# Optimization experiments

Hardware: AMD Instinct MI355X
Metric: run time of the kernel (lower is better)

Reference implementation:

```python
import jax, jax.numpy as jnp
import numpy as np

EMB = 1024
HEAD = 64
RANK = 8
LRA_SCL = 2.0
LORA = 1.0


def setup_inputs() -> dict:
    key = jax.random.key(0)
    ks = jax.random.split(key, 12)
    s = 1.0 / np.sqrt(EMB)
    sr = 1.0 / np.sqrt(RANK)
    inp = {
        "batEmb": jax.random.normal(ks[0], (8, 2048, EMB), dtype=jnp.float32),
        "tokMrk": jax.random.randint(ks[1], (8, 2048), 0, 2, dtype=jnp.int32),
        # base projections, nn.Linear weight layout [out, in]
        "Wq": jax.random.uniform(ks[2], (HEAD, EMB), jnp.float32, -s, s),
        "Wk": jax.random.uniform(ks[3], (HEAD, EMB), jnp.float32, -s, s),
        "Wv": jax.random.uniform(ks[4], (HEAD, EMB), jnp.float32, -s, s),
        # LoRA: A [rank, emb], B [head, rank]. (Original inits B to zero; we
        # randomize with small scale so the LoRA path is numerically exercised.)
        "Aq": jax.random.uniform(ks[5], (RANK, EMB), jnp.float32, -s, s),
        "Bq": jax.random.uniform(ks[6], (HEAD, RANK), jnp.float32, -sr, sr) * 0.02,
        "Ak": jax.random.uniform(ks[7], (RANK, EMB), jnp.float32, -s, s),
        "Bk": jax.random.uniform(ks[8], (HEAD, RANK), jnp.float32, -sr, sr) * 0.02,
        "Av": jax.random.uniform(ks[9], (RANK, EMB), jnp.float32, -s, s),
        "Bv": jax.random.uniform(ks[10], (HEAD, RANK), jnp.float32, -sr, sr) * 0.02,
    }
    return inp


def _proj(x, W, A, B):
    # base + LoRA low-rank delta (dropout = identity in eval)
    base = jnp.einsum('bse,he->bsh', x, W)
    lora = jnp.einsum('bsr,hr->bsh', jnp.einsum('bse,re->bsr', x, A), B)
    return base + lora * (LRA_SCL * LORA)


def reference(batEmb, tokMrk, Wq, Wk, Wv, Aq, Bq, Ak, Bk, Av, Bv):
    q = _proj(batEmb, Wq, Aq, Bq)  # [B,S,H]
    k = _proj(batEmb, Wk, Ak, Bk)
    v = _proj(batEmb, Wv, Av, Bv)
    w = jnp.einsum('bqh,bkh->bqk', q, k) * (HEAD ** -0.5)  # [B,S,S]
    mask = (tokMrk == 0)[:, None, :]  # [B,1,S] over key dim
    w = jnp.where(mask, -jnp.inf, w)
    w = jax.nn.softmax(w, axis=-1)
    w = jnp.nan_to_num(w, nan=0.0)
    return jnp.einsum('bqk,bkh->bqh', w, v)
```

## Files before the change

### kernel.cpp

```cpp
#include <hip/hip_runtime.h>
#include <hip/hip_bf16.h>
#include <stdint.h>

#define EMB 1024
#define NB 8
#define SEQ 2048
#define RANK 8
#define SPLIT 4

#define BM 64
#define BK 64
#define NSTG 16
#define BUFB 32768
#define NBUF 3

typedef __attribute__((ext_vector_type(8))) short bf16x8;
typedef __attribute__((ext_vector_type(4))) float f32x4;
typedef unsigned short u16;
typedef unsigned int u32;

__device__ __forceinline__ u16 f2bf(float f) {
  u32 u = __builtin_bit_cast(u32, f);
  u = (u + 0x7fffu + ((u >> 16) & 1u)) >> 16;
  return (u16)u;
}
__device__ __forceinline__ u32 pk2(float lo, float hi) {
  return (u32)f2bf(lo) | ((u32)f2bf(hi) << 16);
}
__device__ __forceinline__ void gll16(const void* g, void* l) {
  __builtin_amdgcn_global_load_lds(
      (const __attribute__((address_space(1))) unsigned int*)g,
      (__attribute__((address_space(3))) unsigned int*)l, 16, 0, 0);
}

#define PBAR()   asm volatile("s_barrier" ::: "memory")
#define WAITV(n) asm volatile("s_waitcnt vmcnt(" #n ")" ::: "memory")
#define WAITL()  asm volatile("s_waitcnt lgkmcnt(0)" ::: "memory")

__global__ __launch_bounds__(256) void fold_k(
    const float* __restrict__ Wq, const float* __restrict__ Wk, const float* __restrict__ Wv,
    const float* __restrict__ Aq, const float* __restrict__ Bq,
    const float* __restrict__ Ak, const float* __restrict__ Bk,
    const float* __restrict__ Av, const float* __restrict__ Bv,
    u16* __restrict__ weff) {
  int m = blockIdx.x;
  int mat = m >> 6, h = m & 63;
  const float* W = mat == 0 ? Wq : (mat == 1 ? Wk : Wv);
  const float* A = mat == 0 ? Aq : (mat == 1 ? Ak : Av);
  const float* B = mat == 0 ? Bq : (mat == 1 ? Bk : Bv);
  float bb[RANK];
#pragma unroll
  for (int r = 0; r < RANK; r++) bb[r] = 2.0f * B[h * RANK + r];
  int e = threadIdx.x * 4;
  float4 w4 = *(const float4*)(W + h * EMB + e);
  float a0 = w4.x, a1 = w4.y, a2 = w4.z, a3 = w4.w;
#pragma unroll
  for (int r = 0; r < RANK; r++) {
    float4 av = *(const float4*)(A + r * EMB + e);
    a0 += bb[r] * av.x; a1 += bb[r] * av.y; a2 += bb[r] * av.z; a3 += bb[r] * av.w;
  }
  u16* o = weff + (size_t)m * EMB + e;
  o[0] = f2bf(a0); o[1] = f2bf(a1); o[2] = f2bf(a2); o[3] = f2bf(a3);
}

__global__ __launch_bounds__(512) void proj_k(
    const float* __restrict__ X, const u16* __restrict__ weff,
    u16* __restrict__ qws, u16* __restrict__ kws, u16* __restrict__ vws) {
  extern __shared__ __align__(16) char smem[];

  int t = threadIdx.x;
  int w = t >> 6, l = t & 63;
  int rbase = blockIdx.x * BM;

  if (w >= 6) {
    int q = w - 6;
    int p = q * 64 + l;
    int xrow = p & 63;
    int xh = p >> 6;
    const float* xsrc = X + (size_t)(rbase + xrow) * EMB + xh * 8;
    int wkoff = ((l & 7) ^ (l >> 3)) << 3;
    int wc0 = l >> 3;

    float4 xr0[8], xr1[8];

#define ISSUE_X(st, xr) do {                                              \
    const float* s_ = xsrc + (st) * BK;                                   \
    _Pragma("unroll")                                                     \
    for (int wi_ = 0; wi_ < 4; wi_++) {                                   \
      xr[wi_*2]   = *(const float4*)(s_ + wi_ * 16);                      \
      xr[wi_*2+1] = *(const float4*)(s_ + wi_ * 16 + 4);                  \
    } } while (0)

#define WRITE_X(bufp, xr) do {                                            \
    _Pragma("unroll")                                                     \
    for (int wi_ = 0; wi_ < 4; wi_++) {                                   \
      uint4 v_;                                                           \
      v_.x = pk2(xr[wi_*2].x,   xr[wi_*2].y);                             \
      v_.y = pk2(xr[wi_*2].z,   xr[wi_*2].w);                             \
      v_.z = pk2(xr[wi_*2+1].x, xr[wi_*2+1].y);                           \
      v_.w = pk2(xr[wi_*2+1].z, xr[wi_*2+1].w);                           \
      *(uint4*)((bufp) + (wi_*2 + xh) * 1024 + xrow * 16) = v_;           \
    } } while (0)

#define ISSUE_W(st, bufp) do {                                            \
    _Pragma("unroll")                                                     \
    for (int i_ = 0; i_ < 12; i_++) { int wj_ = q * 12 + i_;              \
      gll16(weff + (size_t)(wj_ * 8 + wc0) * EMB + (st) * BK + wkoff,     \
            (bufp) + 8192 + wj_ * 1024);                                  \
    } } while (0)

    ISSUE_X(0, xr0); ISSUE_W(0, smem);
    ISSUE_X(1, xr1); ISSUE_W(1, smem + BUFB);
    WRITE_X(smem, xr0);
    WAITV(20);
    WAITL();

    for (int s = 0; s < NSTG; s++) {
      PBAR();
      char* nbuf = smem + ((s + 2) % NBUF) * BUFB;
      char* wbuf = smem + ((s + 1) % NBUF) * BUFB;
      if ((s & 1) == 0) {
        if (s + 2 < NSTG) { ISSUE_X(s + 2, xr0); ISSUE_W(s + 2, nbuf); }
        if (s + 1 < NSTG) WRITE_X(wbuf, xr1);
      } else {
        if (s + 2 < NSTG) { ISSUE_X(s + 2, xr1); ISSUE_W(s + 2, nbuf); }
        if (s + 1 < NSTG) WRITE_X(wbuf, xr0);
      }
      if (s + 2 < NSTG) { WAITV(20); } else { WAITV(0); }
      WAITL();
    }
#undef ISSUE_X
#undef WRITE_X
#undef ISSUE_W
  } else {
    int l15 = l & 15, lh = l >> 4;
    f32x4 acc[4][2];
    f32x4 zero = {0.f, 0.f, 0.f, 0.f};
#pragma unroll
    for (int rt = 0; rt < 4; rt++)
#pragma unroll
      for (int ct = 0; ct < 2; ct++) acc[rt][ct] = zero;
    int swz = (l15 & 7) << 4;

    for (int s = 0; s < NSTG; s++) {
      PBAR();
      const char* buf = smem + (s % NBUF) * BUFB;
#pragma unroll
      for (int j = 0; j < 2; j++) {
        bf16x8 a[4];
#pragma unroll
        for (int rt = 0; rt < 4; rt++)
          a[rt] = *(const bf16x8*)(buf + (j * 4 + lh) * 1024 + (rt * 16 + l15) * 16);
#pragma unroll
        for (int ct = 0; ct < 2; ct++) {
          int col = (w * 2 + ct) * 16 + l15;
          bf16x8 bf = *(const bf16x8*)(buf + 8192 + col * 128 +
                                       ((j * 64 + lh * 16) ^ swz));
#pragma unroll
          for (int rt = 0; rt < 4; rt++)
            acc[rt][ct] = __builtin_amdgcn_mfma_f32_16x16x32_bf16(a[rt], bf, acc[rt][ct], 0, 0, 0);
        }
      }
    }

#pragma unroll
    for (int rt = 0; rt < 4; rt++)
#pragma unroll
      for (int ct = 0; ct < 2; ct++) {
        int c = (w * 2 + ct) * 16 + l15;
#pragma unroll
        for (int r = 0; r < 4; r++) {
          int rr = rbase + rt * 16 + lh * 4 + r;
          float av = acc[rt][ct][r];
          if (c < 64) av *= 0.125f;
          u16 v = f2bf(av);
          if (c < 64) {
            qws[(size_t)rr * 64 + c] = v;
          } else if (c < 128) {
            kws[(size_t)rr * 64 + (c - 64)] = v;
          } else {
            int bb = rr >> 11, tok = rr & 2047;
            vws[((size_t)(bb * 64 + (c - 128))) * SEQ + tok] = v;
          }
        }
      }
  }
}

__global__ __launch_bounds__(256) void attn_k(
    const u16* __restrict__ qws, const u16* __restrict__ kws, const u16* __restrict__ vws,
    const int* __restrict__ mrk,
    float* __restrict__ po, float* __restrict__ pmp, float* __restrict__ plp) {
  __shared__ __align__(16) u16 ks[2 * 4096];
  __shared__ __align__(16) u16 vt[2 * 4096];
  __shared__ __align__(16) u16 ps[4 * 1024];

  int b = blockIdx.y;
  int z = blockIdx.z;
  int q0 = blockIdx.x * 64;
  int t = threadIdx.x;
  int w = t >> 6, l = t & 63;
  int l15 = l & 15, lh = l >> 4;

  int srow = t >> 3;
  int ssw = (((t & 7) << 4) ^ ((srow & 7) << 4)) >> 1;
  char* ksb = (char*)ks + w * 1024;
  char* vtb = (char*)vt + w * 1024;

  const u16* qp = qws + ((size_t)(b * SEQ + q0 + w * 16 + l15)) * 64 + lh * 8;
  bf16x8 qb0 = *(const bf16x8*)qp;
  bf16x8 qb1 = *(const bf16x8*)(qp + 32);

  f32x4 o[4];
  f32x4 zero = {0.f, 0.f, 0.f, 0.f};
#pragma unroll
  for (int ht = 0; ht < 4; ht++) o[ht] = zero;
  float mrow = -30000.0f, lrow = 0.f;

  int swz = (l15 & 7) << 4;
  int koffA = ((lh << 4) ^ swz) >> 1;
  int koffB = ((64 | (lh << 4)) ^ swz) >> 1;
  u16* psw = ps + w * 1024 + l15 * 64;

  const int NC = SEQ / 64 / SPLIT;
  int kk0 = z * (SEQ / SPLIT);

#define STAGE_KV(buf, kk)                                                          \
  do {                                                                             \
    gll16(kws + ((size_t)(b * SEQ + (kk) + srow)) * 64 + ssw,                      \
          ksb + (buf) * 8192);                                                     \
    gll16(kws + ((size_t)(b * SEQ + (kk) + srow + 32)) * 64 + ssw,                 \
          ksb + (buf) * 8192 + 4096);                                              \
    gll16(vws + ((size_t)(b * 64 + srow)) * SEQ + (kk) + ssw,                      \
          vtb + (buf) * 8192);                                                     \
    gll16(vws + ((size_t)(b * 64 + srow + 32)) * SEQ + (kk) + ssw,                 \
          vtb + (buf) * 8192 + 4096);                                              \
  } while (0)

  STAGE_KV(0, kk0);
  __syncthreads();

  int cur = 0;
  for (int kc = 0; kc < NC; kc++) {
    int kk = kk0 + kc * 64;
    if (kc + 1 < NC) STAGE_KV(cur ^ 1, kk + 64);

    int4 mi[4];
#pragma unroll
    for (int nt = 0; nt < 4; nt++)
      mi[nt] = *(const int4*)(mrk + b * SEQ + kk + nt * 16 + lh * 4);

    const u16* kb = ks + cur * 4096;
    f32x4 sa[4];
#pragma unroll
    for (int nt = 0; nt < 4; nt++) {
      const u16* kr = kb + (nt * 16 + l15) * 64;
      bf16x8 k0 = *(const bf16x8*)(kr + koffA);
      bf16x8 k1 = *(const bf16x8*)(kr + koffB);
      f32x4 s = zero;
      s = __builtin_amdgcn_mfma_f32_16x16x32_bf16(k0, qb0, s, 0, 0, 0);
      s = __builtin_amdgcn_mfma_f32_16x16x32_bf16(k1, qb1, s, 0, 0, 0);
      sa[nt] = s;
    }

    const u16* vbb = vt + cur * 4096;
    bf16x8 vb[4][2];
#pragma unroll
    for (int ht = 0; ht < 4; ht++) {
      const u16* vr = vbb + (ht * 16 + l15) * 64;
      vb[ht][0] = *(const bf16x8*)(vr + koffA);
      vb[ht][1] = *(const bf16x8*)(vr + koffB);
    }

#pragma unroll
    for (int nt = 0; nt < 4; nt++) {
      sa[nt][0] = mi[nt].x ? sa[nt][0] : -INFINITY;
      sa[nt][1] = mi[nt].y ? sa[nt][1] : -INFINITY;
      sa[nt][2] = mi[nt].z ? sa[nt][2] : -INFINITY;
      sa[nt][3] = mi[nt].w ? sa[nt][3] : -INFINITY;
    }
    float t0 = fmaxf(fmaxf(sa[0][0], sa[0][1]), fmaxf(sa[0][2], sa[0][3]));
    float t1 = fmaxf(fmaxf(sa[1][0], sa[1][1]), fmaxf(sa[1][2], sa[1][3]));
    float t2 = fmaxf(fmaxf(sa[2][0], sa[2][1]), fmaxf(sa[2][2], sa[2][3]));
    float t3 = fmaxf(fmaxf(sa[3][0], sa[3][1]), fmaxf(sa[3][2], sa[3][3]));
    float tm = fmaxf(fmaxf(t0, t1), fmaxf(t2, t3));
    tm = fmaxf(tm, __shfl_xor(tm, 16));
    tm = fmaxf(tm, __shfl_xor(tm, 32));

    if (!__all(tm <= mrow + 8.0f)) {
      float nm = fmaxf(mrow, tm);
      float alpha = __expf(mrow - nm);
      mrow = nm;
      lrow *= alpha;
      float a0 = __shfl(alpha, lh * 4 + 0);
      float a1 = __shfl(alpha, lh * 4 + 1);
      float a2 = __shfl(alpha, lh * 4 + 2);
      float a3 = __shfl(alpha, lh * 4 + 3);
#pragma unroll
      for (int ht = 0; ht < 4; ht++) {
        o[ht][0] *= a0; o[ht][1] *= a1; o[ht][2] *= a2; o[ht][3] *= a3;
      }
    }

    float ts = 0.f;
#pragma unroll
    for (int nt = 0; nt < 4; nt++) {
#pragma unroll
      for (int r = 0; r < 4; r++) {
        float p = __expf(sa[nt][r] - mrow);
        sa[nt][r] = p;
        ts += p;
      }
    }
    ts += __shfl_xor(ts, 16);
    ts += __shfl_xor(ts, 32);
    lrow += ts;

#pragma unroll
    for (int nt = 0; nt < 4; nt++) {
      u32 plo = pk2(sa[nt][0], sa[nt][1]);
      u32 phi = pk2(sa[nt][2], sa[nt][3]);
      *(uint2*)&psw[(((nt * 32 + lh * 8) ^ swz) >> 1)] = make_uint2(plo, phi);
    }
    bf16x8 ap0 = *(const bf16x8*)(psw + koffA);
    bf16x8 ap1 = *(const bf16x8*)(psw + koffB);

#pragma unroll
    for (int ht = 0; ht < 4; ht++) {
      o[ht] = __builtin_amdgcn_mfma_f32_16x16x32_bf16(ap0, vb[ht][0], o[ht], 0, 0, 0);
      o[ht] = __builtin_amdgcn_mfma_f32_16x16x32_bf16(ap1, vb[ht][1], o[ht], 0, 0, 0);
    }
    __syncthreads();
    cur ^= 1;
  }
#undef STAGE_KV

#pragma unroll
  for (int r = 0; r < 4; r++) {
    int rr = q0 + w * 16 + lh * 4 + r;
    float* pob = po + ((size_t)z * NB * SEQ + (size_t)b * SEQ + rr) * 64;
#pragma unroll
    for (int ht = 0; ht < 4; ht++) pob[ht * 16 + l15] = o[ht][r];
  }
  if (lh == 0) {
    int rr = q0 + w * 16 + l15;
    pmp[(size_t)z * NB * SEQ + (size_t)b * SEQ + rr] = mrow;
    plp[(size_t)z * NB * SEQ + (size_t)b * SEQ + rr] = lrow;
  }
}

__global__ __launch_bounds__(256) void merge_k(
    const float* __restrict__ po, const float* __restrict__ pmp,
    const float* __restrict__ plp, float* __restrict__ out) {
  int tid = threadIdx.x;
  int row = blockIdx.x * 32 + (tid >> 3);
  int c8 = (tid & 7) * 8;
  const int RT = NB * SEQ;

  float m[SPLIT], lv[SPLIT];
  float M = -INFINITY;
#pragma unroll
  for (int s = 0; s < SPLIT; s++) {
    m[s] = pmp[(size_t)s * RT + row];
    lv[s] = plp[(size_t)s * RT + row];
    M = fmaxf(M, m[s]);
  }
  float o8[8];
#pragma unroll
  for (int j = 0; j < 8; j++) o8[j] = 0.f;
  float L = 0.f;
  if (M != -INFINITY) {
#pragma unroll
    for (int s = 0; s < SPLIT; s++) {
      float ws = __expf(m[s] - M);
      L += ws * lv[s];
      const float* p = po + ((size_t)s * RT + row) * 64 + c8;
#pragma unroll
      for (int j = 0; j < 8; j++) o8[j] += ws * p[j];
    }
  }
  float inv = (L > 0.f) ? 1.0f / L : 0.f;
  float* op = out + (size_t)row * 64 + c8;
#pragma unroll
  for (int j = 0; j < 8; j++) op[j] = o8[j] * inv;
}

extern "C" void kernel_launch(void* const* d_in, const int* in_sizes, int n_in,
                              void* d_out, int out_size, void* d_ws, size_t ws_size,
                              hipStream_t stream) {
  const float* X   = (const float*)d_in[0];
  const int*   mrk = (const int*)d_in[1];
  const float* Wq  = (const float*)d_in[2];
  const float* Wk  = (const float*)d_in[3];
  const float* Wv  = (const float*)d_in[4];
  const float* Aq  = (const float*)d_in[5];
  const float* Bq  = (const float*)d_in[6];
  const float* Ak  = (const float*)d_in[7];
  const float* Bk  = (const float*)d_in[8];
  const float* Av  = (const float*)d_in[9];
  const float* Bv  = (const float*)d_in[10];

  u16* weff = (u16*)d_ws;
  u16* qws  = (u16*)((char*)d_ws + (512 << 10));
  u16* kws  = qws + (size_t)16384 * 64;
  u16* vws  = kws + (size_t)16384 * 64;
  float* po  = (float*)((char*)d_ws + ((size_t)6656 << 10));
  float* pmp = po + (size_t)SPLIT * 16384 * 64;
  float* plp = pmp + (size_t)SPLIT * 16384;

  (void)hipFuncSetAttribute((const void*)proj_k,
                            hipFuncAttributeMaxDynamicSharedMemorySize, NBUF * BUFB);

  fold_k<<<192, 256, 0, stream>>>(Wq, Wk, Wv, Aq, Bq, Ak, Bk, Av, Bv, weff);
  proj_k<<<256, 512, NBUF * BUFB, stream>>>(X, weff, qws, kws, vws);
  attn_k<<<dim3(32, 8, SPLIT), 256, 0, stream>>>(qws, kws, vws, mrk, po, pmp, plp);
  merge_k<<<512, 256, 0, stream>>>(po, pmp, plp, (float*)d_out);
}
```

Baseline: 68.29 us.

## Stream fp32 X directly to LDS via async loads, convert to bf16 in compute waves

The producer waves no longer load X into registers, convert it to bf16 and store it to LDS. They now issue global_load_lds copies of raw fp32 X into a swizzled LDS region, and the MFMA waves convert fp32 to bf16 after reading from LDS. This removes register staging and the LDS write path from the producers and makes the X and W loads uniformly asynchronous. In exchange, LDS use per buffer grows from 32 KB to 40 KB, LDS read traffic in the compute waves doubles for X, and conversion work is added to the MFMA waves.

```diff
diff --git a/kernel.cpp b/kernel.cpp
--- a/kernel.cpp
+++ b/kernel.cpp
@@ -11,7 +11,7 @@
 #define BM 64
 #define BK 64
 #define NSTG 16
-#define BUFB 32768
+#define BUFB 40960
 #define NBUF 3
 
 typedef __attribute__((ext_vector_type(8))) short bf16x8;
@@ -27,6 +27,10 @@
 __device__ __forceinline__ u32 pk2(float lo, float hi) {
   return (u32)f2bf(lo) | ((u32)f2bf(hi) << 16);
 }
+__device__ __forceinline__ u32 cvtpk(float lo, float hi) {
+  __hip_bfloat162 h = __float22bfloat162_rn(make_float2(lo, hi));
+  u32 u; __builtin_memcpy(&u, &h, 4); return u;
+}
 __device__ __forceinline__ void gll16(const void* g, void* l) {
   __builtin_amdgcn_global_load_lds(
       (const __attribute__((address_space(1))) unsigned int*)g,
@@ -35,7 +39,6 @@
 
 #define PBAR()   asm volatile("s_barrier" ::: "memory")
 #define WAITV(n) asm volatile("s_waitcnt vmcnt(" #n ")" ::: "memory")
-#define WAITL()  asm volatile("s_waitcnt lgkmcnt(0)" ::: "memory")
 
 __global__ __launch_bounds__(256) void fold_k(
     const float* __restrict__ Wq, const float* __restrict__ Wk, const float* __restrict__ Wv,
@@ -74,64 +77,38 @@
 
   if (w >= 6) {
     int q = w - 6;
-    int p = q * 64 + l;
-    int xrow = p & 63;
-    int xh = p >> 6;
-    const float* xsrc = X + (size_t)(rbase + xrow) * EMB + xh * 8;
-    int wkoff = ((l & 7) ^ (l >> 3)) << 3;
+    int wkoff = ((l & 7) ^ (l >> 3)) * 8;
     int wc0 = l >> 3;
-
-    float4 xr0[8], xr1[8];
-
-#define ISSUE_X(st, xr) do {                                              \
-    const float* s_ = xsrc + (st) * BK;                                   \
-    _Pragma("unroll")                                                     \
-    for (int wi_ = 0; wi_ < 4; wi_++) {                                   \
-      xr[wi_*2]   = *(const float4*)(s_ + wi_ * 16);                      \
-      xr[wi_*2+1] = *(const float4*)(s_ + wi_ * 16 + 4);                  \
+    int lr4 = l >> 4;
+    int l15 = l & 15;
+
+#define ISSUE(st, bufp) do {                                                   \
+    _Pragma("unroll")                                                          \
+    for (int i_ = 0; i_ < 8; i_++) {                                           \
+      int rrel_ = q * 32 + i_ * 4 + lr4;                                       \
+      int xo_ = 4 * (l15 ^ (rrel_ & 7));        \
+      gll16(X + (size_t)(rbase + rrel_) * EMB + (st) * BK + xo_,               \
+            (bufp) + q * 8192 + i_ * 1024);                                    \
+    }                                                                          \
+    _Pragma("unroll")                                                          \
+    for (int i_ = 0; i_ < 12; i_++) { int wj_ = q * 12 + i_;                   \
+      gll16(weff + (size_t)(wj_ * 8 + wc0) * EMB + (st) * BK + wkoff,          \
+            (bufp) + 16384 + wj_ * 1024);                                      \
     } } while (0)
 
-#define WRITE_X(bufp, xr) do {                                            \
-    _Pragma("unroll")                                                     \
-    for (int wi_ = 0; wi_ < 4; wi_++) {                                   \
-      uint4 v_;                                                           \
-      v_.x = pk2(xr[wi_*2].x,   xr[wi_*2].y);                             \
-      v_.y = pk2(xr[wi_*2].z,   xr[wi_*2].w);                             \
-      v_.z = pk2(xr[wi_*2+1].x, xr[wi_*2+1].y);                           \
-      v_.w = pk2(xr[wi_*2+1].z, xr[wi_*2+1].w);                           \
-      *(uint4*)((bufp) + (wi_*2 + xh) * 1024 + xrow * 16) = v_;           \
-    } } while (0)
-
-#define ISSUE_W(st, bufp) do {                                            \
-    _Pragma("unroll")                                                     \
-    for (int i_ = 0; i_ < 12; i_++) { int wj_ = q * 12 + i_;              \
-      gll16(weff + (size_t)(wj_ * 8 + wc0) * EMB + (st) * BK + wkoff,     \
-            (bufp) + 8192 + wj_ * 1024);                                  \
-    } } while (0)
-
-    ISSUE_X(0, xr0); ISSUE_W(0, smem);
-    ISSUE_X(1, xr1); ISSUE_W(1, smem + BUFB);
-    WRITE_X(smem, xr0);
+    ISSUE(0, smem);
+    ISSUE(1, smem + BUFB);
     WAITV(20);
-    WAITL();
-
     for (int s = 0; s < NSTG; s++) {
       PBAR();
-      char* nbuf = smem + ((s + 2) % NBUF) * BUFB;
-      char* wbuf = smem + ((s + 1) % NBUF) * BUFB;
-      if ((s & 1) == 0) {
-        if (s + 2 < NSTG) { ISSUE_X(s + 2, xr0); ISSUE_W(s + 2, nbuf); }
-        if (s + 1 < NSTG) WRITE_X(wbuf, xr1);
-      } else {
-        if (s + 2 < NSTG) { ISSUE_X(s + 2, xr1); ISSUE_W(s + 2, nbuf); }
-        if (s + 1 < NSTG) WRITE_X(wbuf, xr0);
+      if (s + 2 < NSTG) {
+        ISSUE(s + 2, smem + ((s + 2) % NBUF) * BUFB);
+        WAITV(20);
+      } else if (s + 1 < NSTG) {
+        WAITV(0);
       }
-      if (s + 2 < NSTG) { WAITV(20); } else { WAITV(0); }
-      WAITL();
-    }
-#undef ISSUE_X
-#undef WRITE_X
-#undef ISSUE_W
+    }
+#undef ISSUE
   } else {
     int l15 = l & 15, lh = l >> 4;
     f32x4 acc[4][2];
@@ -140,22 +117,31 @@
     for (int rt = 0; rt < 4; rt++)
 #pragma unroll
       for (int ct = 0; ct < 2; ct++) acc[rt][ct] = zero;
-    int swz = (l15 & 7) << 4;
 
     for (int s = 0; s < NSTG; s++) {
       PBAR();
-      const char* buf = smem + (s % NBUF) * BUFB;
+      const char* bx = smem + (s % NBUF) * BUFB;
+      const char* bw = bx + 16384;
 #pragma unroll
       for (int j = 0; j < 2; j++) {
         bf16x8 a[4];
 #pragma unroll
-        for (int rt = 0; rt < 4; rt++)
-          a[rt] = *(const bf16x8*)(buf + (j * 4 + lh) * 1024 + (rt * 16 + l15) * 16);
+        for (int rt = 0; rt < 4; rt++) {
+          int r = rt * 16 + l15;
+          int sw = (r & 7) << 4;
+          const char* base = bx + r * 256;
+          f32x4 lo = *(const f32x4*)(base + ((j * 128 + lh * 32) ^ sw));
+          f32x4 hi = *(const f32x4*)(base + ((j * 128 + lh * 32 + 16) ^ sw));
+          union { bf16x8 v; u32 u[4]; } au;
+          au.u[0] = cvtpk(lo.x, lo.y); au.u[1] = cvtpk(lo.z, lo.w);
+          au.u[2] = cvtpk(hi.x, hi.y); au.u[3] = cvtpk(hi.z, hi.w);
+          a[rt] = au.v;
+        }
 #pragma unroll
         for (int ct = 0; ct < 2; ct++) {
           int col = (w * 2 + ct) * 16 + l15;
-          bf16x8 bf = *(const bf16x8*)(buf + 8192 + col * 128 +
-                                       ((j * 64 + lh * 16) ^ swz));
+          bf16x8 bf = *(const bf16x8*)(bw + col * 128 +
+                                       ((j * 64 + lh * 16) ^ ((col & 7) << 4)));
 #pragma unroll
           for (int rt = 0; rt < 4; rt++)
             acc[rt][ct] = __builtin_amdgcn_mfma_f32_16x16x32_bf16(a[rt], bf, acc[rt][ct], 0, 0, 0);
```

Measured after the change: 61.67 us. -9.7%, faster.
